# Optimization experiments

Hardware: AMD Instinct MI355X
Metric: run time of the kernel (lower is better)

The kernel has to match this reference:

```python
import jax, jax.numpy as jnp
import numpy as np

EPS = 1e-5

def _ternary_ste(w):
    # STEQuantize: round(w/scale) clamped to [-1,1]; straight-through gradient.
    scale = jnp.maximum(jnp.mean(jnp.abs(w)), EPS)
    q = jnp.clip(jnp.round(w / scale), -1.0, 1.0)
    return w + jax.lax.stop_gradient(q - w)

def _bitlinear(x, w):
    # BitLinear: y = x @ (ternary(w) * scale)^T, scale = mean|w| (differentiable).
    scale = jnp.maximum(jnp.mean(jnp.abs(w)), EPS)
    return x @ (_ternary_ste(w) * scale).T

def _op_library(x, indices, weights, ops):
    # ops: (n_ops, D, D). Per-op ternary quantize + scale, then one batched einsum
    # instead of the python loop of small matmuls.
    n_ops = ops.shape[0]
    scales = jnp.maximum(jnp.mean(jnp.abs(ops), axis=(1, 2)), EPS)  # (n_ops,)
    q = jnp.clip(jnp.round(ops / scales[:, None, None]), -1.0, 1.0)
    w_eff = (ops + jax.lax.stop_gradient(q - ops)) * scales[:, None, None]  # (n,o,d)
    # transformed[n] = x @ w_eff[n]^T  ->  (B, S, n_ops, D)
    T = jnp.einsum('bsd,nod->bsno', x, w_eff)
    out = (1e-5 / n_ops) * jnp.sum(T, axis=2)
    gathered = jnp.take_along_axis(T, indices[:, :, :, None], axis=2)  # (B,S,K,D)
    out = out + jnp.sum(weights[..., None] * gathered, axis=2)
    return out

def _mem_read(x, slots, W_read):
    d = slots.shape[1]
    key = x @ W_read.T
    attn = jax.nn.softmax(key @ slots.T / jnp.sqrt(jnp.float32(d)), axis=-1)
    return attn @ slots

def _layernorm(x, gamma, beta):
    mu = jnp.mean(x, axis=-1, keepdims=True)
    var = jnp.var(x, axis=-1, keepdims=True)
    return (x - mu) * jax.lax.rsqrt(var + EPS) * gamma + beta

def _single_pass(reason, ops, W_router, slots, W_read, W_mix, ln_gamma, ln_beta, top_k):
    logits = _bitlinear(reason, W_router)              # (B,S,n_ops)
    vals, indices = jax.lax.top_k(logits, top_k)       # (B,S,K)
    weights = jax.nn.softmax(vals, axis=-1)
    op_out = _op_library(reason, indices, weights, ops)
    mem_out = _mem_read(reason, slots, W_read)
    mixed = jnp.concatenate([op_out, mem_out], axis=-1) @ W_mix.T
    return _layernorm(reason + mixed, ln_gamma, ln_beta)

def _write_signal(q, slots, W_wk, W_wg, W_wv):
    d = slots.shape[1]
    wk = q @ W_wk.T
    wg = jax.nn.sigmoid(q @ W_wg.T)                    # (B,S,1)
    wv = q @ W_wv.T
    addr = jax.nn.softmax(wk @ slots.T / jnp.sqrt(jnp.float32(d)), axis=-1)
    return wg * wv + 0.1 * (addr @ slots)

def setup_inputs() -> dict:
    key = jax.random.key(0)
    ks = jax.random.split(key, 12)
    B, S, d_model, d_reason = 8, 2048, 1024, 128
    n_ops, n_slots = 32, 16
    return {
        'hidden': jax.random.normal(ks[0], (B, S, d_model), jnp.float32),
        'force_depth': 2,
        'W_down': jax.random.normal(ks[1], (d_reason, d_model), jnp.float32) * 0.02,
        'W_up': jax.random.normal(ks[2], (d_model, d_reason), jnp.float32) * 0.02,
        'ops': jax.random.normal(ks[3], (n_ops, d_reason, d_reason), jnp.float32) * 0.02,
        'W_router': jax.random.normal(ks[4], (n_ops, d_reason), jnp.float32) * 0.02,
        'slots': jax.random.normal(ks[5], (n_slots, d_reason), jnp.float32) * 0.01,
        'W_read': jax.random.normal(ks[6], (d_reason, d_reason), jnp.float32) * 0.02,
        'W_wk': jax.random.normal(ks[7], (d_reason, d_reason), jnp.float32) * 0.02,
        'W_wg': jax.random.normal(ks[8], (1, d_reason), jnp.float32) * 0.02,
        'W_wv': jax.random.normal(ks[9], (d_reason, d_reason), jnp.float32) * 0.02,
        'W_mix': jax.random.normal(ks[10], (d_reason, 2 * d_reason), jnp.float32) * 0.02,
        'ln_gamma': jnp.ones((d_reason,), jnp.float32),
        'ln_beta': jnp.zeros((d_reason,), jnp.float32),
        'write_scale': jnp.float32(0.01),
    }

def reference(hidden, force_depth, W_down, W_up, ops, W_router, slots, W_read,
              W_wk, W_wg, W_wv, W_mix, ln_gamma, ln_beta, write_scale):
    top_k = 2
    reason = _bitlinear(hidden, W_down)
    for _ in range(int(force_depth)):
        reason = _single_pass(reason, ops, W_router, slots, W_read, W_mix,
                              ln_gamma, ln_beta, top_k)
    reason = reason + write_scale * _write_signal(reason, slots, W_wk, W_wg, W_wv)
    out = _bitlinear(reason, W_up)
    return hidden + out
```

## Files before the change

kernel.cpp:

```cpp
#include <hip/hip_runtime.h>


#define DR   128
#define DM   1024
#define NTOK 16384
#define NOPS 32
#define COEF (1e-5f / 32.f)

typedef __attribute__((ext_vector_type(8))) short bfrag;
typedef __attribute__((ext_vector_type(4))) float f32x4;

__device__ __forceinline__ ushort f2b_bits(float f) {
  union { float f; uint i; } c; c.f = f;
  uint x = c.i;
  return (ushort)((x + 0x7fffu + ((x >> 16) & 1u)) >> 16);
}
__device__ __forceinline__ float qeff(float w, float s) {
  float q = rintf(w / s);
  q = fminf(1.f, fmaxf(-1.f, q));
  return q * s;
}
__device__ __forceinline__ float waveRed(float v) {
#pragma unroll
  for (int m = 32; m > 0; m >>= 1) v += __shfl_xor(v, m, 64);
  return v;
}

#define OFF_SUMS    0
#define OFF_OPSSC   256
#define OFF_WDE     512
#define OFF_WUE     (OFF_WDE + 262144)
#define OFF_WRT     (OFF_WUE + 262144)
#define OFF_OPSB    (OFF_WRT + 16384)
#define OFF_WMIXA   (OFF_OPSB + 1048576)
#define OFF_WWVB    (OFF_WMIXA + 32768)
#define OFF_MRS     (OFF_WWVB + 32768)
#define OFF_MWS     (OFF_MRS + 8192)
#define OFF_SB      (OFF_MWS + 8192)
#define OFF_SLOTS   (OFF_SB + 8192)
#define OFF_WWG     (OFF_SLOTS + 8192)
#define OFF_GAMMA   (OFF_WWG + 512)
#define OFF_BETA    (OFF_GAMMA + 512)
#define OFF_WSC     (OFF_BETA + 512)
#define OFF_RF      (OFF_WSC + 256)
#define WS_TOTAL    (OFF_RF + 4194304)

__global__ __launch_bounds__(1024) void k_absum_all(
    const float* __restrict__ W_down, const float* __restrict__ W_router,
    const float* __restrict__ W_up, const float* __restrict__ ops,
    float* __restrict__ sums) {
  __shared__ float ws16[16];
  const int y = blockIdx.x;
  const int tid = threadIdx.x;
  const float* src; int n;
  if (y == 0)      { src = W_down;   n = 131072; }
  else if (y == 1) { src = W_router; n = 4096;   }
  else if (y == 2) { src = W_up;     n = 131072; }
  else             { src = ops + (size_t)(y - 3) * 16384; n = 16384; }
  float s = 0.f;
  for (int i = tid * 4; i < n; i += 4096) {
    float4 v = *(const float4*)(src + i);
    s += fabsf(v.x) + fabsf(v.y) + fabsf(v.z) + fabsf(v.w);
  }
  s = waveRed(s);
  const int lane = tid & 63, wv = tid >> 6;
  if (lane == 0) ws16[wv] = s;
  __syncthreads();
  if (tid == 0) {
    float t = 0.f;
#pragma unroll
    for (int i = 0; i < 16; ++i) t += ws16[i];
    sums[y] = t;
  }
}

__global__ __launch_bounds__(256) void k_build(
    const float* __restrict__ W_down, const float* __restrict__ W_up,
    const float* __restrict__ W_router, const float* __restrict__ ops,
    const float* __restrict__ W_read, const float* __restrict__ W_wk,
    const float* __restrict__ W_wg, const float* __restrict__ W_wv,
    const float* __restrict__ W_mix, const float* __restrict__ slots,
    const float* __restrict__ gamma, const float* __restrict__ beta,
    const float* __restrict__ wscale, int has_wsc, const float* __restrict__ sums,
    ushort* __restrict__ WdE, ushort* __restrict__ WuE, float* __restrict__ WrT,
    ushort* __restrict__ opsB, float* __restrict__ opsScale,
    ushort* __restrict__ WmixA, ushort* __restrict__ WwvB,
    float* __restrict__ Mrs, float* __restrict__ Mws, float* __restrict__ SBw,
    float* __restrict__ slotsF, float* __restrict__ WwgF,
    float* __restrict__ gammaF, float* __restrict__ betaF, float* __restrict__ wscF) {
  int id = blockIdx.x * 256 + threadIdx.x;
  const float s_wd = fmaxf(sums[0] * (1.f / 131072.f), 1e-5f);
  const float s_wr = fmaxf(sums[1] * (1.f / 4096.f), 1e-5f);
  const float s_wu = fmaxf(sums[2] * (1.f / 131072.f), 1e-5f);

  if (id < 131072) { WdE[id] = f2b_bits(qeff(W_down[id], s_wd)); return; }
  id -= 131072;
  if (id < 131072) { WuE[id] = f2b_bits(qeff(W_up[id], s_wu)); return; }
  id -= 131072;
  if (id < 4096) {
    int d = id >> 5, n = id & 31;
    WrT[id] = qeff(W_router[n * DR + d], s_wr);
    return;
  }
  id -= 4096;
  if (id < 524288) {
    int n = id >> 14;
    float s = fmaxf(sums[3 + n] * (1.f / 16384.f), 1e-5f);
    float q = rintf(ops[id] / s);
    q = fminf(1.f, fmaxf(-1.f, q));
    opsB[id] = f2b_bits(q);
    return;
  }
  id -= 524288;
  if (id < 32) { opsScale[id] = fmaxf(sums[3 + id] * (1.f / 16384.f), 1e-5f); return; }
  id -= 32;
  if (id < 16384) {
    int r = id >> 7, o = id & 127;
    WmixA[id] = f2b_bits(W_mix[r * 256 + o]);
    return;
  }
  id -= 16384;
  if (id < 16384) { WwvB[id] = f2b_bits(W_wv[id]); return; }
  id -= 16384;
  if (id < 2048) {
    int d = id >> 4, j = id & 15;
    float a = 0.f;
#pragma unroll 8
    for (int o = 0; o < DR; ++o) a += W_read[o * DR + d] * slots[j * DR + o];
    Mrs[id] = a;
    return;
  }
  id -= 2048;
  if (id < 2048) {
    int d = id >> 4, j = id & 15;
    float a = 0.f;
#pragma unroll 8
    for (int o = 0; o < DR; ++o) a += W_wk[o * DR + d] * slots[j * DR + o];
    Mws[id] = a;
    return;
  }
  id -= 2048;
  if (id < 2048) {
    int j = id >> 7, r = id & 127;
    float a = 0.f;
#pragma unroll 8
    for (int o = 0; o < DR; ++o) a += slots[j * DR + o] * W_mix[r * 256 + 128 + o];
    SBw[id] = a;
    return;
  }
  id -= 2048;
  if (id < 2048) { slotsF[id] = slots[id]; return; }
  id -= 2048;
  if (id < 128) { WwgF[id] = W_wg[id]; return; }
  id -= 128;
  if (id < 128) { gammaF[id] = gamma[id]; return; }
  id -= 128;
  if (id < 128) { betaF[id] = beta[id]; return; }
  id -= 128;
  if (id == 0) { wscF[0] = has_wsc ? wscale[0] : 0.01f; }
}

__global__ __launch_bounds__(512) void k_down(const float* __restrict__ hidden,
                                              const ushort* __restrict__ WdE,
                                              float* __restrict__ X) {
  __shared__ ushort stg[64][136];

  const int tid = threadIdx.x;
  const int w = tid >> 6, lane = tid & 63;
  const int quad = lane >> 4, mrow = lane & 15;
  const int t0 = blockIdx.x * 64;

  f32x4 dacc[4];
#pragma unroll
  for (int m = 0; m < 4; ++m) dacc[m] = (f32x4){0.f, 0.f, 0.f, 0.f};

  for (int kc = 0; kc < 8; ++kc) {
    for (int i = tid; i < 2048; i += 512) {
      int t = i >> 5, c = (i & 31) * 4;
      float4 v = *(const float4*)(hidden + (size_t)(t0 + t) * DM + kc * 128 + c);
      stg[t][c] = f2b_bits(v.x); stg[t][c + 1] = f2b_bits(v.y);
      stg[t][c + 2] = f2b_bits(v.z); stg[t][c + 3] = f2b_bits(v.w);
    }
    __syncthreads();
#pragma unroll
    for (int kt = 0; kt < 4; ++kt) {
      bfrag b = *(const bfrag*)(WdE + (size_t)(w * 16 + mrow) * DM + kc * 128 + kt * 32 + quad * 8);
#pragma unroll
      for (int m = 0; m < 4; ++m) {
        bfrag a = *(const bfrag*)&stg[m * 16 + mrow][kt * 32 + quad * 8];
        dacc[m] = __builtin_amdgcn_mfma_f32_16x16x32_bf16(a, b, dacc[m], 0, 0, 0);
      }
    }
    __syncthreads();
  }
#pragma unroll
  for (int m = 0; m < 4; ++m)
#pragma unroll
    for (int r = 0; r < 4; ++r)
      X[(size_t)(t0 + m * 16 + quad * 4 + r) * DR + w * 16 + mrow] = dacc[m][r];
}

__global__ __launch_bounds__(512) void k_pass2(
    float* __restrict__ X, ushort* __restrict__ RF, int emit,
    const float* __restrict__ WrT, const ushort* __restrict__ opsB,
    const float* __restrict__ opsScale, const ushort* __restrict__ WmixA,
    const float* __restrict__ Mrs, const float* __restrict__ SBw,
    const float* __restrict__ gammaF, const float* __restrict__ betaF,
    const ushort* __restrict__ WwvB, const float* __restrict__ Mws,
    const float* __restrict__ slotsF, const float* __restrict__ WwgF,
    const float* __restrict__ wscF) {
  __shared__ float  xsf[64][132];
  __shared__ ushort xsb[64][136];
  __shared__ float  lg[64][33];
  __shared__ float  coefT[32][64];
  __shared__ float  attn[64][17];
  __shared__ float  at2[64][17];
  __shared__ float  WrTs[4096];
  __shared__ float  Mrss[2048];
  __shared__ float  Mwss[2048];
  __shared__ float  SBws[2048];
  __shared__ float  slotss[2048];
  __shared__ int    seli[64][2];
  __shared__ float  selw[64][2];
  __shared__ float  gp[64];
  __shared__ float  partS[8][4][4];
  __shared__ float  partQ[8][4][4];

  const int tid = threadIdx.x;
  const int w = tid >> 6, lane = tid & 63;
  const int quad = lane >> 4, mrow = lane & 15;
  const int t0 = blockIdx.x * 64;

  {
    float4* d;
    const float4* s;
    d = (float4*)WrTs; s = (const float4*)WrT;
    for (int i = tid; i < 1024; i += 512) d[i] = s[i];
    ((float4*)Mrss)[tid]   = ((const float4*)Mrs)[tid];
    ((float4*)Mwss)[tid]   = ((const float4*)Mws)[tid];
    ((float4*)SBws)[tid]   = ((const float4*)SBw)[tid];
    ((float4*)slotss)[tid] = ((const float4*)slotsF)[tid];
  }
  for (int i = tid; i < 2048; i += 512) {
    float4 v = *(const float4*)(X + (size_t)t0 * DR + i * 4);
    int t = i >> 5, c = (i & 31) * 4;
    xsf[t][c] = v.x; xsf[t][c + 1] = v.y; xsf[t][c + 2] = v.z; xsf[t][c + 3] = v.w;
    xsb[t][c] = f2b_bits(v.x); xsb[t][c + 1] = f2b_bits(v.y);
    xsb[t][c + 2] = f2b_bits(v.z); xsb[t][c + 3] = f2b_bits(v.w);
  }
  __syncthreads();

  for (int p = tid; p < 2048; p += 512) {
    int t = p >> 5, n = p & 31;
    const float4* xr = (const float4*)&xsf[t][0];
    float a = 0.f;
#pragma unroll 8
    for (int d4 = 0; d4 < 32; ++d4) {
      float4 x = xr[d4];
      a += x.x * WrTs[(d4 * 4 + 0) * 32 + n];
      a += x.y * WrTs[(d4 * 4 + 1) * 32 + n];
      a += x.z * WrTs[(d4 * 4 + 2) * 32 + n];
      a += x.w * WrTs[(d4 * 4 + 3) * 32 + n];
    }
    lg[t][n] = a;
  }
  for (int p = tid; p < 1024; p += 512) {
    int t = p >> 4, j = p & 15;
    const float4* xr = (const float4*)&xsf[t][0];
    float a = 0.f;
#pragma unroll 8
    for (int d4 = 0; d4 < 32; ++d4) {
      float4 x = xr[d4];
      a += x.x * Mrss[(d4 * 4 + 0) * 16 + j];
      a += x.y * Mrss[(d4 * 4 + 1) * 16 + j];
      a += x.z * Mrss[(d4 * 4 + 2) * 16 + j];
      a += x.w * Mrss[(d4 * 4 + 3) * 16 + j];
    }
    attn[t][j] = a * 0.088388347648318447f;
  }
  __syncthreads();

  if (tid < 64) {
    float v0 = -1e30f; int i0 = 0;
#pragma unroll
    for (int n = 0; n < 32; ++n) { float v = lg[tid][n]; if (v > v0) { v0 = v; i0 = n; } }
    float v1 = -1e30f; int i1 = 0;
#pragma unroll
    for (int n = 0; n < 32; ++n)
      if (n != i0) { float v = lg[tid][n]; if (v > v1) { v1 = v; i1 = n; } }
    float e = expf(v1 - v0);
    float w0 = 1.f / (1.f + e);
    seli[tid][0] = i0; seli[tid][1] = i1;
    selw[tid][0] = w0; selw[tid][1] = e * w0;
  } else if (tid < 128) {
    const int t = tid - 64;
    float m = -1e30f;
#pragma unroll
    for (int j = 0; j < 16; ++j) m = fmaxf(m, attn[t][j]);
    float s = 0.f;
#pragma unroll
    for (int j = 0; j < 16; ++j) { float ee = expf(attn[t][j] - m); attn[t][j] = ee; s += ee; }
    float inv = 1.f / s;
#pragma unroll
    for (int j = 0; j < 16; ++j) attn[t][j] *= inv;
  }
  __syncthreads();

  for (int p = tid; p < 2048; p += 512) {
    int n = p >> 6, t = p & 63;
    float cf = COEF;
    if (n == seli[t][0]) cf += selw[t][0];
    if (n == seli[t][1]) cf += selw[t][1];
    coefT[n][t] = cf * opsScale[n];
  }
  __syncthreads();

  bfrag a[4][4];
#pragma unroll
  for (int m = 0; m < 4; ++m)
#pragma unroll
    for (int kt = 0; kt < 4; ++kt)
      a[m][kt] = *(const bfrag*)&xsb[m * 16 + mrow][kt * 32 + quad * 8];

  const ushort* Bp = opsB + (size_t)(w * 16 + mrow) * DR + quad * 8;
  bfrag bc[4], bn[4];
#pragma unroll
  for (int kt = 0; kt < 4; ++kt) bc[kt] = *(const bfrag*)(Bp + kt * 32);

  f32x4 out[4];
#pragma unroll
  for (int m = 0; m < 4; ++m) out[m] = (f32x4){0.f, 0.f, 0.f, 0.f};

  for (int n = 0; n < NOPS; ++n) {
    if (n + 1 < NOPS) {
      const ushort* Bn = Bp + (size_t)(n + 1) * (DR * DR);
#pragma unroll
      for (int kt = 0; kt < 4; ++kt) bn[kt] = *(const bfrag*)(Bn + kt * 32);
    }
    f32x4 tmp[4];
#pragma unroll
    for (int m = 0; m < 4; ++m) tmp[m] = (f32x4){0.f, 0.f, 0.f, 0.f};
#pragma unroll
    for (int kt = 0; kt < 4; ++kt)
#pragma unroll
      for (int m = 0; m < 4; ++m)
        tmp[m] = __builtin_amdgcn_mfma_f32_16x16x32_bf16(a[m][kt], bc[kt], tmp[m], 0, 0, 0);
#pragma unroll
    for (int m = 0; m < 4; ++m) {
      f32x4 cf = *(const f32x4*)&coefT[n][m * 16 + quad * 4];
      out[m] += cf * tmp[m];
    }
    if (n + 1 < NOPS) {
#pragma unroll
      for (int kt = 0; kt < 4; ++kt) bc[kt] = bn[kt];
    }
  }
  __syncthreads();

#pragma unroll
  for (int m = 0; m < 4; ++m)
#pragma unroll
    for (int r = 0; r < 4; ++r)
      xsb[m * 16 + quad * 4 + r][w * 16 + mrow] = f2b_bits(out[m][r]);
  __syncthreads();

  const int mtile = w & 3;
  const int ch = (w >> 2) * 64;
  {
    bfrag a2[4];
#pragma unroll
    for (int kt = 0; kt < 4; ++kt)
      a2[kt] = *(const bfrag*)&xsb[mtile * 16 + mrow][kt * 32 + quad * 8];

    f32x4 acc[4];
#pragma unroll
    for (int i = 0; i < 4; ++i) acc[i] = (f32x4){0.f, 0.f, 0.f, 0.f};
#pragma unroll
    for (int kt = 0; kt < 4; ++kt)
#pragma unroll
      for (int nt = 0; nt < 4; ++nt) {
        bfrag b = *(const bfrag*)(WmixA + (size_t)(ch + nt * 16 + mrow) * DR + kt * 32 + quad * 8);
        acc[nt] = __builtin_amdgcn_mfma_f32_16x16x32_bf16(a2[kt], b, acc[nt], 0, 0, 0);
      }

    float v[4][4];
#pragma unroll
    for (int nt = 0; nt < 4; ++nt) {
      const int col = ch + nt * 16 + mrow;
#pragma unroll
      for (int r = 0; r < 4; ++r) {
        const int t = mtile * 16 + quad * 4 + r;
        float y0 = 0.f;
#pragma unroll
        for (int j = 0; j < 16; ++j) y0 += attn[t][j] * SBws[j * 128 + col];
        v[nt][r] = acc[nt][r] + xsf[t][col] + y0;
      }
    }
    float s[4], q[4];
#pragma unroll
    for (int r = 0; r < 4; ++r) {
      float ps = 0.f, pq = 0.f;
#pragma unroll
      for (int nt = 0; nt < 4; ++nt) { ps += v[nt][r]; pq += v[nt][r] * v[nt][r]; }
      s[r] = ps; q[r] = pq;
    }
#pragma unroll
    for (int m = 1; m < 16; m <<= 1)
#pragma unroll
      for (int r = 0; r < 4; ++r) {
        s[r] += __shfl_xor(s[r], m, 64);
        q[r] += __shfl_xor(q[r], m, 64);
      }
    if (mrow == 0)
#pragma unroll
      for (int r = 0; r < 4; ++r) { partS[w][quad][r] = s[r]; partQ[w][quad][r] = q[r]; }
    __syncthreads();

    float mu[4], rsd[4];
#pragma unroll
    for (int r = 0; r < 4; ++r) {
      float ts = s[r] + partS[w ^ 4][quad][r];
      float tq = q[r] + partQ[w ^ 4][quad][r];
      mu[r] = ts * (1.f / DR);
      float var = tq * (1.f / DR) - mu[r] * mu[r];
      rsd[r] = rsqrtf(var + 1e-5f);
    }
    if (!emit) {
#pragma unroll
      for (int nt = 0; nt < 4; ++nt) {
        const int col = ch + nt * 16 + mrow;
        const float g = gammaF[col], bb = betaF[col];
#pragma unroll
        for (int r = 0; r < 4; ++r) {
          const int t = mtile * 16 + quad * 4 + r;
          X[(size_t)(t0 + t) * DR + col] = (v[nt][r] - mu[r]) * rsd[r] * g + bb;
        }
      }
      return;
    }
#pragma unroll
    for (int nt = 0; nt < 4; ++nt) {
      const int col = ch + nt * 16 + mrow;
      const float g = gammaF[col], bb = betaF[col];
#pragma unroll
      for (int r = 0; r < 4; ++r) {
        const int t = mtile * 16 + quad * 4 + r;
        float val = (v[nt][r] - mu[r]) * rsd[r] * g + bb;
        xsf[t][col] = val;
        xsb[t][col] = f2b_bits(val);
      }
    }
  }
  __syncthreads();

  for (int p = tid; p < 1024; p += 512) {
    int t = p >> 4, j = p & 15;
    const float4* xr = (const float4*)&xsf[t][0];
    float a2 = 0.f;
#pragma unroll 8
    for (int d4 = 0; d4 < 32; ++d4) {
      float4 x = xr[d4];
      a2 += x.x * Mwss[(d4 * 4 + 0) * 16 + j];
      a2 += x.y * Mwss[(d4 * 4 + 1) * 16 + j];
      a2 += x.z * Mwss[(d4 * 4 + 2) * 16 + j];
      a2 += x.w * Mwss[(d4 * 4 + 3) * 16 + j];
    }
    at2[t][j] = a2 * 0.088388347648318447f;
  }
  __syncthreads();

  if (tid < 64) {
    const float4* xr = (const float4*)&xsf[tid][0];
    float z = 0.f;
#pragma unroll 8
    for (int d4 = 0; d4 < 32; ++d4) {
      float4 x = xr[d4];
      z += x.x * WwgF[d4 * 4 + 0] + x.y * WwgF[d4 * 4 + 1]
         + x.z * WwgF[d4 * 4 + 2] + x.w * WwgF[d4 * 4 + 3];
    }
    gp[tid] = wscF[0] / (1.f + expf(-z));
  } else if (tid < 128) {
    const int t = tid - 64;
    float m = -1e30f;
#pragma unroll
    for (int j = 0; j < 16; ++j) m = fmaxf(m, at2[t][j]);
    float s = 0.f;
#pragma unroll
    for (int j = 0; j < 16; ++j) { float e = expf(at2[t][j] - m); at2[t][j] = e; s += e; }
    float inv = 1.f / s;
#pragma unroll
    for (int j = 0; j < 16; ++j) at2[t][j] *= inv;
  }
  __syncthreads();

  {
    bfrag a2[4];
#pragma unroll
    for (int kt = 0; kt < 4; ++kt)
      a2[kt] = *(const bfrag*)&xsb[mtile * 16 + mrow][kt * 32 + quad * 8];

    f32x4 acc[4];
#pragma unroll
    for (int i = 0; i < 4; ++i) acc[i] = (f32x4){0.f, 0.f, 0.f, 0.f};
#pragma unroll
    for (int kt = 0; kt < 4; ++kt)
#pragma unroll
      for (int nt = 0; nt < 4; ++nt) {
        bfrag b = *(const bfrag*)(WwvB + (size_t)(ch + nt * 16 + mrow) * DR + kt * 32 + quad * 8);
        acc[nt] = __builtin_amdgcn_mfma_f32_16x16x32_bf16(a2[kt], b, acc[nt], 0, 0, 0);
      }

    const float c01 = wscF[0] * 0.1f;
#pragma unroll
    for (int nt = 0; nt < 4; ++nt) {
      const int col = ch + nt * 16 + mrow;
#pragma unroll
      for (int r = 0; r < 4; ++r) {
        const int t = mtile * 16 + quad * 4 + r;
        float mo = 0.f;
#pragma unroll
        for (int j = 0; j < 16; ++j) mo += at2[t][j] * slotss[j * DR + col];
        float val = xsf[t][col] + gp[t] * acc[nt][r] + c01 * mo;
        RF[(size_t)(t0 + t) * DR + col] = f2b_bits(val);
      }
    }
  }
}

__global__ __launch_bounds__(256) void k_up(const ushort* __restrict__ Rf,
                                            const ushort* __restrict__ WuE,
                                            const float* __restrict__ hidden,
                                            float* __restrict__ out) {
  __shared__ float cs[64][132];

  const int wave = threadIdx.x >> 6, lane = threadIdx.x & 63;
  const int quad = lane >> 4, mrow = lane & 15;
  const int mt = blockIdx.x >> 3, ngrp = blockIdx.x & 7;
  const int m0b = mt * 64;
  const int m0 = m0b + wave * 16;
  const int c0 = ngrp * 128;

  f32x4 acc[8];
#pragma unroll
  for (int i = 0; i < 8; ++i) acc[i] = (f32x4){0.f, 0.f, 0.f, 0.f};

  const ushort* Ap = Rf + (size_t)(m0 + mrow) * DR + quad * 8;
#pragma unroll
  for (int kt = 0; kt < 4; ++kt) {
    bfrag a = *(const bfrag*)(Ap + kt * 32);
#pragma unroll
    for (int nt = 0; nt < 8; ++nt) {
      const ushort* Bp = WuE + (size_t)(c0 + nt * 16 + mrow) * DR + kt * 32 + quad * 8;
      bfrag b = *(const bfrag*)Bp;
      acc[nt] = __builtin_amdgcn_mfma_f32_16x16x32_bf16(a, b, acc[nt], 0, 0, 0);
    }
  }
#pragma unroll
  for (int nt = 0; nt < 8; ++nt)
#pragma unroll
    for (int r = 0; r < 4; ++r)
      cs[wave * 16 + quad * 4 + r][nt * 16 + mrow] = acc[nt][r];
  __syncthreads();

#pragma unroll
  for (int k = 0; k < 8; ++k) {
    const int i = threadIdx.x + k * 256;
    const int t = i >> 5, c4 = (i & 31) * 4;
    const size_t idx = (size_t)(m0b + t) * DM + c0 + c4;
    float4 h = *(const float4*)(hidden + idx);
    float4 v;
    v.x = h.x + cs[t][c4];
    v.y = h.y + cs[t][c4 + 1];
    v.z = h.z + cs[t][c4 + 2];
    v.w = h.w + cs[t][c4 + 3];
    *(float4*)(out + idx) = v;
  }
}

extern "C" void kernel_launch(void* const* d_in, const int* in_sizes, int n_in,
                              void* d_out, int out_size, void* d_ws, size_t ws_size,
                              hipStream_t stream) {
  int ns[20]; int nn = 0; int lastsc = -1;
  for (int i = 0; i < n_in; ++i) {
    if (in_sizes[i] == 1) lastsc = i;
    else if (nn < 20) ns[nn++] = i;
  }
  int iH = 0, iWd = 2, iWu = 3, iOps = 4, iWr = 5, iSl = 6, iRe = 7,
      iWk = 8, iWg = 9, iWv = 10, iMx = 11, iG = 12, iB = 13;
  if (nn >= 13) {
    iH  = ns[0];  iWd = ns[1];  iWu = ns[2];  iOps = ns[3]; iWr = ns[4];
    iSl = ns[5];  iRe = ns[6];  iWk = ns[7];  iWg = ns[8];  iWv = ns[9];
    iMx = ns[10]; iG  = ns[11]; iB  = ns[12];
  }
  const float* hidden   = (const float*)d_in[iH];
  const float* W_down   = (const float*)d_in[iWd];
  const float* W_up     = (const float*)d_in[iWu];
  const float* opsw     = (const float*)d_in[iOps];
  const float* W_router = (const float*)d_in[iWr];
  const float* slots    = (const float*)d_in[iSl];
  const float* W_read   = (const float*)d_in[iRe];
  const float* W_wk     = (const float*)d_in[iWk];
  const float* W_wg     = (const float*)d_in[iWg];
  const float* W_wv     = (const float*)d_in[iWv];
  const float* W_mix    = (const float*)d_in[iMx];
  const float* lng      = (const float*)d_in[iG];
  const float* lnb      = (const float*)d_in[iB];
  const float* wscale   = (lastsc >= 0) ? (const float*)d_in[lastsc] : (const float*)d_in[iG];
  const int has_wsc     = (lastsc >= 0) ? 1 : 0;

  char* ws = (char*)d_ws;
  float*  sums   = (float*)(ws + OFF_SUMS);
  float*  opsSc  = (float*)(ws + OFF_OPSSC);
  ushort* WdE    = (ushort*)(ws + OFF_WDE);
  ushort* WuE    = (ushort*)(ws + OFF_WUE);
  float*  WrT    = (float*)(ws + OFF_WRT);
  ushort* opsB   = (ushort*)(ws + OFF_OPSB);
  ushort* WmixA  = (ushort*)(ws + OFF_WMIXA);
  ushort* WwvB   = (ushort*)(ws + OFF_WWVB);
  float*  Mrs    = (float*)(ws + OFF_MRS);
  float*  Mws    = (float*)(ws + OFF_MWS);
  float*  SBw    = (float*)(ws + OFF_SB);
  float*  slotsF = (float*)(ws + OFF_SLOTS);
  float*  WwgF   = (float*)(ws + OFF_WWG);
  float*  gammaF = (float*)(ws + OFF_GAMMA);
  float*  betaF  = (float*)(ws + OFF_BETA);
  float*  wscF   = (float*)(ws + OFF_WSC);
  ushort* RF     = (ushort*)(ws + OFF_RF);

  float* X = (float*)d_out;

  k_absum_all<<<35, 1024, 0, stream>>>(W_down, W_router, W_up, opsw, sums);
  k_build<<<3250, 256, 0, stream>>>(W_down, W_up, W_router, opsw, W_read, W_wk, W_wg,
                                    W_wv, W_mix, slots, lng, lnb, wscale, has_wsc,
                                    sums, WdE, WuE, WrT, opsB, opsSc, WmixA, WwvB,
                                    Mrs, Mws, SBw, slotsF, WwgF, gammaF, betaF, wscF);
  k_down<<<256, 512, 0, stream>>>(hidden, WdE, X);
  k_pass2<<<256, 512, 0, stream>>>(X, RF, 0, WrT, opsB, opsSc, WmixA, Mrs, SBw,
                                   gammaF, betaF, WwvB, Mws, slotsF, WwgF, wscF);
  k_pass2<<<256, 512, 0, stream>>>(X, RF, 1, WrT, opsB, opsSc, WmixA, Mrs, SBw,
                                   gammaF, betaF, WwvB, Mws, slotsF, WwgF, wscF);
  k_up<<<2048, 256, 0, stream>>>(RF, WuE, hidden, X);
}
```

Baseline: 344.0 us.

## Split abs-sum reduction across blocks with atomics; stage k_up A tile in LDS

The weight abs-sum kernel now spreads each tensor over 8 blocks of 256 threads using scalar loads and atomicAdd into a zeroed sums buffer, which requires an extra memset launch. Separately, k_up loads the 64x128 bf16 activation tile into shared memory with coalesced vector loads and reads the per-wave A fragments from LDS, replacing strided direct global fragment loads. The changes aim to increase parallelism in the tiny reduction and improve coalescing in the up projection. Float atomics make the sum order nondeterministic, and the LDS staging adds two barriers.

```diff
diff --git a/kernel.cpp b/kernel.cpp
--- a/kernel.cpp
+++ b/kernel.cpp
@@ -45,33 +45,25 @@
 #define OFF_RF      (OFF_WSC + 256)
 #define WS_TOTAL    (OFF_RF + 4194304)
 
-__global__ __launch_bounds__(1024) void k_absum_all(
+__global__ __launch_bounds__(256) void k_absum_all(
     const float* __restrict__ W_down, const float* __restrict__ W_router,
     const float* __restrict__ W_up, const float* __restrict__ ops,
     float* __restrict__ sums) {
-  __shared__ float ws16[16];
-  const int y = blockIdx.x;
-  const int tid = threadIdx.x;
-  const float* src; int n;
-  if (y == 0)      { src = W_down;   n = 131072; }
-  else if (y == 1) { src = W_router; n = 4096;   }
-  else if (y == 2) { src = W_up;     n = 131072; }
-  else             { src = ops + (size_t)(y - 3) * 16384; n = 16384; }
+  __shared__ float ws4[4];
+  const int y = blockIdx.y;
+  const float* src; int n; float* dst;
+  if (y == 0)      { src = W_down;   n = 131072; dst = &sums[0]; }
+  else if (y == 1) { src = W_router; n = 4096;   dst = &sums[1]; }
+  else if (y == 2) { src = W_up;     n = 131072; dst = &sums[2]; }
+  else { src = ops + (size_t)(y - 3) * 16384; n = 16384; dst = &sums[y]; }
   float s = 0.f;
-  for (int i = tid * 4; i < n; i += 4096) {
-    float4 v = *(const float4*)(src + i);
-    s += fabsf(v.x) + fabsf(v.y) + fabsf(v.z) + fabsf(v.w);
-  }
+  for (int i = blockIdx.x * 256 + threadIdx.x; i < n; i += 8 * 256)
+    s += fabsf(src[i]);
   s = waveRed(s);
-  const int lane = tid & 63, wv = tid >> 6;
-  if (lane == 0) ws16[wv] = s;
-  __syncthreads();
-  if (tid == 0) {
-    float t = 0.f;
-#pragma unroll
-    for (int i = 0; i < 16; ++i) t += ws16[i];
-    sums[y] = t;
-  }
+  int lane = threadIdx.x & 63, wv = threadIdx.x >> 6;
+  if (lane == 0) ws4[wv] = s;
+  __syncthreads();
+  if (threadIdx.x == 0) atomicAdd(dst, ws4[0] + ws4[1] + ws4[2] + ws4[3]);
 }
 
 __global__ __launch_bounds__(256) void k_build(
@@ -532,27 +524,37 @@
                                             const float* __restrict__ hidden,
                                             float* __restrict__ out) {
   __shared__ float cs[64][132];
+  ushort (*stg)[136] = reinterpret_cast<ushort(*)[136]>(&cs[0][0]);
 
   const int wave = threadIdx.x >> 6, lane = threadIdx.x & 63;
   const int quad = lane >> 4, mrow = lane & 15;
   const int mt = blockIdx.x >> 3, ngrp = blockIdx.x & 7;
   const int m0b = mt * 64;
-  const int m0 = m0b + wave * 16;
   const int c0 = ngrp * 128;
 
+  for (int i = threadIdx.x; i < 1024; i += 256) {
+    const int r = i >> 4, c = (i & 15) * 8;
+    *(bfrag*)&stg[r][c] = *(const bfrag*)(Rf + (size_t)(m0b + r) * DR + c);
+  }
+  __syncthreads();
+
+  bfrag a[4];
+#pragma unroll
+  for (int kt = 0; kt < 4; ++kt)
+    a[kt] = *(const bfrag*)&stg[wave * 16 + mrow][kt * 32 + quad * 8];
+  __syncthreads();
+
   f32x4 acc[8];
 #pragma unroll
   for (int i = 0; i < 8; ++i) acc[i] = (f32x4){0.f, 0.f, 0.f, 0.f};
 
-  const ushort* Ap = Rf + (size_t)(m0 + mrow) * DR + quad * 8;
 #pragma unroll
   for (int kt = 0; kt < 4; ++kt) {
-    bfrag a = *(const bfrag*)(Ap + kt * 32);
 #pragma unroll
     for (int nt = 0; nt < 8; ++nt) {
       const ushort* Bp = WuE + (size_t)(c0 + nt * 16 + mrow) * DR + kt * 32 + quad * 8;
       bfrag b = *(const bfrag*)Bp;
-      acc[nt] = __builtin_amdgcn_mfma_f32_16x16x32_bf16(a, b, acc[nt], 0, 0, 0);
+      acc[nt] = __builtin_amdgcn_mfma_f32_16x16x32_bf16(a[kt], b, acc[nt], 0, 0, 0);
     }
   }
 #pragma unroll
@@ -629,7 +631,8 @@
 
   float* X = (float*)d_out;
 
-  k_absum_all<<<35, 1024, 0, stream>>>(W_down, W_router, W_up, opsw, sums);
+  hipMemsetAsync(ws + OFF_SUMS, 0, 256, stream);
+  k_absum_all<<<dim3(8, 35), 256, 0, stream>>>(W_down, W_router, W_up, opsw, sums);
   k_build<<<3250, 256, 0, stream>>>(W_down, W_up, W_router, opsw, W_read, W_wk, W_wg,
                                     W_wv, W_mix, slots, lng, lnb, wscale, has_wsc,
                                     sums, WdE, WuE, WrT, opsB, opsSc, WmixA, WwvB,
```

Result: slower. 351.7 us (+2.2%).
